# Kernel tuning notes

Hardware: AMD Instinct MI355X
Metric: run time of the kernel (lower is better)

## Reference

```python
import jax, jax.numpy as jnp
import numpy as np

H = 2048        # hidden_size
E = 64          # num_experts
TOPK = 4        # top_k_experts
EPS = 1e-6      # rms_norm_eps
SW = 1024       # sliding_window
NEG = jnp.finfo(jnp.float32).min


def setup_inputs() -> dict:
    key = jax.random.key(0)
    k1, k2, k3, k4, k5 = jax.random.split(key, 5)
    B, S = 2, 4096
    x = jax.random.normal(k1, (B, S, H), jnp.float32)
    # 1-based document ids packed contiguously; 0 = padding
    packed_seq_ids = jnp.sort(jax.random.randint(k2, (B, S), 0, 5), axis=-1)
    # 0 = text, 1/2 = vision tokens
    mm_token_type_ids = jax.random.randint(k3, (B, S), 0, 3)
    scale = jax.random.uniform(k4, (H,), jnp.float32, 0.5, 1.5)
    proj_w = jax.random.normal(k5, (E, H), jnp.float32) * 0.02
    return dict(x=x, packed_seq_ids=packed_seq_ids,
                mm_token_type_ids=mm_token_type_ids, scale=scale, proj_w=proj_w)


def _vision_group_ids(mm):
    # per-image-block ids for vision tokens, -1 for text/padding
    is_v = (mm == 1) | (mm == 2)
    is_prev = jnp.concatenate([jnp.zeros_like(is_v[:, :1]), is_v[:, :-1]], axis=-1)
    starts = is_v & ~is_prev
    gid = jnp.cumsum(starts.astype(jnp.int32), axis=1) - 1
    return jnp.where(is_v, gid, -1)


def _build_masks(packed, mm, sliding_window):
    B, S = packed.shape
    pos = jnp.arange(S)
    causal = pos[None, :, None] >= pos[None, None, :]          # [1,S,S] kv<=q
    valid_q = packed[:, :, None] > 0
    valid_kv = packed[:, None, :] > 0
    same_doc = (packed[:, :, None] == packed[:, None, :]) & valid_q & valid_kv
    full = same_doc & causal                                   # [B,S,S]
    sliding = full & ((pos[None, :, None] - pos[None, None, :]) < sliding_window)
    gid = _vision_group_ids(mm)
    same_vg = (gid[:, :, None] == gid[:, None, :]) & (gid[:, :, None] >= 0)
    sliding = (sliding | same_vg) & same_doc
    # additive format, [B,1,S,S]
    full_add = jnp.where(full[:, None], jnp.float32(0.0), NEG)
    sliding_add = jnp.where(sliding[:, None], jnp.float32(0.0), NEG)
    return full_add, sliding_add


def _gate(x, scale, proj_w):
    # Gemma4Gate: RMSNorm(no scale) -> H**-0.5 -> learnable scale -> linear
    #             -> softmax -> top-k -> renormalize
    xf = x.reshape(-1, H)                                      # [N,H]
    xn = xf * jax.lax.rsqrt(jnp.mean(xf * xf, axis=-1, keepdims=True) + EPS)
    xn = xn * (H ** -0.5) * scale
    logits = jnp.einsum('nh,eh->ne', xn, proj_w)               # [N,E]
    probs = jax.nn.softmax(logits, axis=-1)
    weights, indices = jax.lax.top_k(probs, TOPK)              # [N,K]
    weights = weights / jnp.maximum(jnp.sum(weights, axis=-1, keepdims=True), 1e-20)
    return weights, indices


def reference(x, packed_seq_ids, mm_token_type_ids, scale, proj_w):
    full_mask, sliding_mask = _build_masks(packed_seq_ids, mm_token_type_ids, SW)
    weights, indices = _gate(x, scale, proj_w)
    return full_mask, sliding_mask, weights, indices
```

## Files before the change

### kernel.cpp

```cpp
#include <hip/hip_runtime.h>
#include <math.h>

#define S 4096
#define HH 2048
#define NE 64
#define SW 1024
#define MASKED 0xFBFFu

typedef unsigned short u16;
typedef unsigned int u32;

__device__ __align__(16) int g_gid[2 * S];
__device__ __align__(16) float g_pw2[NE * HH];

__device__ __forceinline__ float h2f(u32 lo16) {
    union { u16 u; _Float16 h; } v; v.u = (u16)lo16; return (float)v.h;
}
__device__ __forceinline__ u16 f2h(float f) {
    union { u16 u; _Float16 h; } v; v.h = (_Float16)f; return v.u;
}
__device__ __forceinline__ void u4_to_f8(uint4 v, float* o) {
    o[0] = h2f(v.x & 0xFFFFu); o[1] = h2f(v.x >> 16);
    o[2] = h2f(v.y & 0xFFFFu); o[3] = h2f(v.y >> 16);
    o[4] = h2f(v.z & 0xFFFFu); o[5] = h2f(v.z >> 16);
    o[6] = h2f(v.w & 0xFFFFu); o[7] = h2f(v.w >> 16);
}

__global__ __launch_bounds__(256) void pre_kernel(const int* __restrict__ mm,
                                                  const u16* __restrict__ proj_w) {
    const int blk = blockIdx.x;
    const int t = threadIdx.x;
    if (blk < 2) {
        __shared__ int ts[256];
        const int* m = mm + blk * S;
        const int base_pos = t * 16;
        int vals[16];
#pragma unroll
        for (int i = 0; i < 16; i++) vals[i] = m[base_pos + i];
        bool prevv = false;
        if (base_pos > 0) {
            int pv = m[base_pos - 1];
            prevv = (pv == 1) || (pv == 2);
        }
        int cnt = 0;
        {
            bool pv = prevv;
#pragma unroll
            for (int i = 0; i < 16; i++) {
                bool is = (vals[i] == 1) || (vals[i] == 2);
                cnt += (is && !pv) ? 1 : 0;
                pv = is;
            }
        }
        ts[t] = cnt;
        __syncthreads();
        for (int off = 1; off < 256; off <<= 1) {
            int add = (t >= off) ? ts[t - off] : 0;
            __syncthreads();
            ts[t] += add;
            __syncthreads();
        }
        int base = ts[t] - cnt;
        {
            bool pv = prevv;
            int run = base;
#pragma unroll
            for (int i = 0; i < 16; i++) {
                bool is = (vals[i] == 1) || (vals[i] == 2);
                run += (is && !pv) ? 1 : 0;
                g_gid[blk * S + base_pos + i] = is ? (run - 1) : -1;
                pv = is;
            }
        }
    } else {
        int idx = (blk - 2) * 256 + t;
        int e = idx >> 11;
        int h = idx & 2047;
        g_pw2[(h >> 2) * 256 + e * 4 + (h & 3)] = h2f((u32)proj_w[idx]);
    }
}

__global__ __launch_bounds__(256) void fused_kernel(
    const u16* __restrict__ x, const u16* __restrict__ scale,
    const int* __restrict__ packed,
    u16* __restrict__ full_out, u16* __restrict__ slid_out,
    u16* __restrict__ w_out, u16* __restrict__ i_out) {

    __shared__ float factor[16];
    __shared__ float xs[16][132];
    __shared__ float part[4][16][65];

    const int t = threadIdx.x;

    if (blockIdx.x >= 512) {
        const int tid = (blockIdx.x - 512) * 256 + t;
        const int kc = tid & 511;
        const int q = (tid >> 9) & 4095;
        const int b = tid >> 21;
        const int k0 = kc * 8;

        const int pq = packed[b * S + q];
        const int gq = g_gid[b * S + q];
        const int4 pk0 = *(const int4*)(packed + b * S + k0);
        const int4 pk1 = *(const int4*)(packed + b * S + k0 + 4);
        const int4 gk0 = *(const int4*)(g_gid + b * S + k0);
        const int4 gk1 = *(const int4*)(g_gid + b * S + k0 + 4);

        int pkj[8] = {pk0.x, pk0.y, pk0.z, pk0.w, pk1.x, pk1.y, pk1.z, pk1.w};
        int gkj[8] = {gk0.x, gk0.y, gk0.z, gk0.w, gk1.x, gk1.y, gk1.z, gk1.w};
        u32 fm[8], sm[8];
#pragma unroll
        for (int j = 0; j < 8; j++) {
            int k = k0 + j;
            bool sd = (pq > 0) && (pkj[j] == pq);
            bool fl = sd && (q >= k);
            bool sl = ((fl && ((q - k) < SW)) || ((gkj[j] == gq) && (gq >= 0))) && sd;
            fm[j] = fl ? 0u : MASKED;
            sm[j] = sl ? 0u : MASKED;
        }
        uint4 f4, s4;
        f4.x = fm[0] | (fm[1] << 16); f4.y = fm[2] | (fm[3] << 16);
        f4.z = fm[4] | (fm[5] << 16); f4.w = fm[6] | (fm[7] << 16);
        s4.x = sm[0] | (sm[1] << 16); s4.y = sm[2] | (sm[3] << 16);
        s4.z = sm[4] | (sm[5] << 16); s4.w = sm[6] | (sm[7] << 16);

        size_t off = (size_t)b * ((size_t)S * S) + (size_t)q * S + k0;
        *(uint4*)(full_out + off) = f4;
        *(uint4*)(slid_out + off) = s4;
        return;
    }

    const int w = t >> 6;
    const int l = t & 63;
    const int tok0 = blockIdx.x * 16;

    for (int tt = w; tt < 16; tt += 4) {
        const uint4* xp = (const uint4*)(x + (size_t)(tok0 + tt) * HH);
        float ss = 0.0f;
#pragma unroll
        for (int j = 0; j < 4; j++) {
            float o[8];
            u4_to_f8(xp[l + 64 * j], o);
#pragma unroll
            for (int i = 0; i < 8; i++) ss += o[i] * o[i];
        }
        for (int off = 32; off >= 1; off >>= 1) ss += __shfl_xor(ss, off);
        if (l == 0)
            factor[tt] = rsqrtf(ss * (1.0f / 2048.0f) + 1e-6f) * 0.022097086912079608f;
    }
    __syncthreads();

    const int g = l & 15;
    const int ts = l >> 4;
    float acc[4][4];
#pragma unroll
    for (int a = 0; a < 4; a++)
#pragma unroll
        for (int bb = 0; bb < 4; bb++) acc[a][bb] = 0.0f;

    const int stok = t >> 4;
    const int sh = (t & 15) * 8;
    const u16* xrow = x + (size_t)(tok0 + stok) * HH + sh;

    uint4 xv_p = *(const uint4*)(xrow);
    uint4 sv_p = *(const uint4*)(scale + sh);

    for (int ch = 0; ch < 16; ch++) {
        __syncthreads();
        {
            float xo[8], so[8];
            u4_to_f8(xv_p, xo);
            u4_to_f8(sv_p, so);
            float fac = factor[stok];
            float4 a, b;
            a.x = xo[0] * fac * so[0]; a.y = xo[1] * fac * so[1];
            a.z = xo[2] * fac * so[2]; a.w = xo[3] * fac * so[3];
            b.x = xo[4] * fac * so[4]; b.y = xo[5] * fac * so[5];
            b.z = xo[6] * fac * so[6]; b.w = xo[7] * fac * so[7];
            *(float4*)&xs[stok][sh] = a;
            *(float4*)&xs[stok][sh + 4] = b;
        }
        __syncthreads();
        if (ch < 15) {
            xv_p = *(const uint4*)(xrow + (ch + 1) * 128);
            sv_p = *(const uint4*)(scale + (ch + 1) * 128 + sh);
        }

        const float* pwb = g_pw2 + (size_t)(ch * 32 + w * 8) * 256 + g * 16;
#pragma unroll
        for (int i = 0; i < 8; i++) {
            float4 p[4];
#pragma unroll
            for (int ej = 0; ej < 4; ej++)
                p[ej] = *(const float4*)(pwb + (size_t)i * 256 + ej * 4);
#pragma unroll
            for (int tk = 0; tk < 4; tk++) {
                float4 xv = *(const float4*)&xs[4 * ts + tk][w * 32 + i * 4];
#pragma unroll
                for (int ej = 0; ej < 4; ej++)
                    acc[tk][ej] += p[ej].x * xv.x + p[ej].y * xv.y +
                                   p[ej].z * xv.z + p[ej].w * xv.w;
            }
        }
    }

#pragma unroll
    for (int tk = 0; tk < 4; tk++)
#pragma unroll
        for (int ej = 0; ej < 4; ej++)
            part[w][4 * ts + tk][4 * g + ej] = acc[tk][ej];
    __syncthreads();

    {
        int tok = t >> 4;
        int eg = t & 15;
        float lg[4];
#pragma unroll
        for (int j = 0; j < 4; j++) {
            int e = eg * 4 + j;
            lg[j] = part[0][tok][e] + part[1][tok][e] + part[2][tok][e] + part[3][tok][e];
        }
        *(float4*)&xs[tok][eg * 4] = make_float4(lg[0], lg[1], lg[2], lg[3]);
    }
    __syncthreads();

    if (t < 16) {
        unsigned long long used = 0ull;
        float bv[4];
        int bi[4];
#pragma unroll
        for (int p = 0; p < 4; p++) {
            float best = -INFINITY;
            int besti = 0;
            for (int e = 0; e < NE; e++) {
                if (used & (1ull << e)) continue;
                float v = xs[t][e];
                if (v > best) { best = v; besti = e; }
            }
            used |= 1ull << besti;
            bv[p] = best;
            bi[p] = besti;
        }
        float ww[4];
        float ssum = 0.0f;
#pragma unroll
        for (int p = 0; p < 4; p++) { ww[p] = expf(bv[p] - bv[0]); ssum += ww[p]; }
        int n = tok0 + t;
#pragma unroll
        for (int p = 0; p < 4; p++) {
            w_out[n * 4 + p] = f2h(ww[p] / ssum);
            i_out[n * 4 + p] = f2h((float)bi[p]);
        }
    }
}

extern "C" void kernel_launch(void* const* d_in, const int* in_sizes, int n_in,
                              void* d_out, int out_size, void* d_ws, size_t ws_size,
                              hipStream_t stream) {
    const u16* x = (const u16*)d_in[0];
    const int* packed = (const int*)d_in[1];
    const int* mm = (const int*)d_in[2];
    const u16* scale = (const u16*)d_in[3];
    const u16* proj_w = (const u16*)d_in[4];

    u16* out = (u16*)d_out;
    u16* full_out = out;
    u16* slid_out = out + 33554432;
    u16* w_out = out + 67108864;
    u16* i_out = out + 67141632;

    pre_kernel<<<514, 256, 0, stream>>>(mm, proj_w);
    fused_kernel<<<512 + 16384, 256, 0, stream>>>(x, scale, packed,
                                                  full_out, slid_out, w_out, i_out);
    (void)in_sizes; (void)n_in; (void)out_size; (void)d_ws; (void)ws_size;
}
```

Measured before the change: 361.5 us.

## Compute gate logits with fp16 MFMA and fold scale into pre-packed weights

The gate GEMM moves from scalar fp32 FMA through shared-memory tiles to 16x16x32 fp16 MFMA instructions, with 64 tokens per block instead of 16. The learnable scale is folded into the projection weights in the pre-kernel, which now stores them as fp16 in an MFMA-friendly B layout. The RMS factor is computed alongside the MFMA loop and applied to the logits afterwards. This removes most shared-memory staging and syncs from the gate path, at the cost of rounding the scaled weights to fp16 and more work per top-k thread. The gate is a small share of the runtime next to the mask writes.

```diff
diff --git a/kernel.cpp b/kernel.cpp
--- a/kernel.cpp
+++ b/kernel.cpp
@@ -9,25 +9,23 @@
 
 typedef unsigned short u16;
 typedef unsigned int u32;
+typedef _Float16 f16;
+typedef f16 f16x8 __attribute__((ext_vector_type(8)));
+typedef float f32x4 __attribute__((ext_vector_type(4)));
 
 __device__ __align__(16) int g_gid[2 * S];
-__device__ __align__(16) float g_pw2[NE * HH];
+__device__ __align__(16) u16 g_pwB[NE * HH];
 
 __device__ __forceinline__ float h2f(u32 lo16) {
-    union { u16 u; _Float16 h; } v; v.u = (u16)lo16; return (float)v.h;
+    union { u16 u; f16 h; } v; v.u = (u16)lo16; return (float)v.h;
 }
 __device__ __forceinline__ u16 f2h(float f) {
-    union { u16 u; _Float16 h; } v; v.h = (_Float16)f; return v.u;
-}
-__device__ __forceinline__ void u4_to_f8(uint4 v, float* o) {
-    o[0] = h2f(v.x & 0xFFFFu); o[1] = h2f(v.x >> 16);
-    o[2] = h2f(v.y & 0xFFFFu); o[3] = h2f(v.y >> 16);
-    o[4] = h2f(v.z & 0xFFFFu); o[5] = h2f(v.z >> 16);
-    o[6] = h2f(v.w & 0xFFFFu); o[7] = h2f(v.w >> 16);
+    union { u16 u; f16 h; } v; v.h = (f16)f; return v.u;
 }
 
 __global__ __launch_bounds__(256) void pre_kernel(const int* __restrict__ mm,
-                                                  const u16* __restrict__ proj_w) {
+                                                  const u16* __restrict__ proj_w,
+                                                  const u16* __restrict__ scale) {
     const int blk = blockIdx.x;
     const int t = threadIdx.x;
     if (blk < 2) {
@@ -76,24 +74,27 @@
         int idx = (blk - 2) * 256 + t;
         int e = idx >> 11;
         int h = idx & 2047;
-        g_pw2[(h >> 2) * 256 + e * 4 + (h & 3)] = h2f((u32)proj_w[idx]);
+        float v = h2f((u32)proj_w[idx]) * h2f((u32)scale[h]);
+        int ch2 = h >> 5;
+        int lrow = (h >> 3) & 3;
+        int j = h & 7;
+        int eg = e >> 4;
+        int ecol = e & 15;
+        g_pwB[(size_t)(((ch2 * 4 + eg) * 64) + lrow * 16 + ecol) * 8 + j] = f2h(v);
     }
 }
 
 __global__ __launch_bounds__(256) void fused_kernel(
-    const u16* __restrict__ x, const u16* __restrict__ scale,
-    const int* __restrict__ packed,
+    const u16* __restrict__ x, const int* __restrict__ packed,
     u16* __restrict__ full_out, u16* __restrict__ slid_out,
     u16* __restrict__ w_out, u16* __restrict__ i_out) {
 
-    __shared__ float factor[16];
-    __shared__ float xs[16][132];
-    __shared__ float part[4][16][65];
+    __shared__ float lg[64][65];
 
     const int t = threadIdx.x;
 
-    if (blockIdx.x >= 512) {
-        const int tid = (blockIdx.x - 512) * 256 + t;
+    if (blockIdx.x >= 128) {
+        const int tid = (blockIdx.x - 128) * 256 + t;
         const int kc = tid & 511;
         const int q = (tid >> 9) & 4095;
         const int b = tid >> 21;
@@ -132,99 +133,54 @@
 
     const int w = t >> 6;
     const int l = t & 63;
-    const int tok0 = blockIdx.x * 16;
-
-    for (int tt = w; tt < 16; tt += 4) {
-        const uint4* xp = (const uint4*)(x + (size_t)(tok0 + tt) * HH);
-        float ss = 0.0f;
-#pragma unroll
-        for (int j = 0; j < 4; j++) {
-            float o[8];
-            u4_to_f8(xp[l + 64 * j], o);
-#pragma unroll
-            for (int i = 0; i < 8; i++) ss += o[i] * o[i];
-        }
-        for (int off = 32; off >= 1; off >>= 1) ss += __shfl_xor(ss, off);
-        if (l == 0)
-            factor[tt] = rsqrtf(ss * (1.0f / 2048.0f) + 1e-6f) * 0.022097086912079608f;
+    const int tok0 = blockIdx.x * 64;
+    const int m16 = l & 15;
+    const int kq = l >> 4;
+
+    const uint4* ap = (const uint4*)(x + (size_t)(tok0 + w * 16 + m16) * HH);
+    const uint4* bp = (const uint4*)g_pwB;
+
+    f32x4 acc0 = {0.f, 0.f, 0.f, 0.f};
+    f32x4 acc1 = {0.f, 0.f, 0.f, 0.f};
+    f32x4 acc2 = {0.f, 0.f, 0.f, 0.f};
+    f32x4 acc3 = {0.f, 0.f, 0.f, 0.f};
+    float ss = 0.0f;
+
+#pragma unroll 4
+    for (int ch2 = 0; ch2 < 64; ++ch2) {
+        union { uint4 u; f16x8 h; } a, b0, b1, b2, b3;
+        a.u = ap[ch2 * 4 + kq];
+        b0.u = bp[(ch2 * 4 + 0) * 64 + l];
+        b1.u = bp[(ch2 * 4 + 1) * 64 + l];
+        b2.u = bp[(ch2 * 4 + 2) * 64 + l];
+        b3.u = bp[(ch2 * 4 + 3) * 64 + l];
+#pragma unroll
+        for (int j = 0; j < 8; j++) {
+            float xf = (float)a.h[j];
+            ss += xf * xf;
+        }
+        acc0 = __builtin_amdgcn_mfma_f32_16x16x32_f16(a.h, b0.h, acc0, 0, 0, 0);
+        acc1 = __builtin_amdgcn_mfma_f32_16x16x32_f16(a.h, b1.h, acc1, 0, 0, 0);
+        acc2 = __builtin_amdgcn_mfma_f32_16x16x32_f16(a.h, b2.h, acc2, 0, 0, 0);
+        acc3 = __builtin_amdgcn_mfma_f32_16x16x32_f16(a.h, b3.h, acc3, 0, 0, 0);
+    }
+
+    ss += __shfl_xor(ss, 16);
+    ss += __shfl_xor(ss, 32);
+    float fac = rsqrtf(ss * (1.0f / 2048.0f) + 1e-6f) * 0.022097086912079608f;
+
+#pragma unroll
+    for (int r = 0; r < 4; r++) {
+        int m = 4 * kq + r;
+        float fm = __shfl(fac, m);
+        lg[w * 16 + m][0 + m16]  = acc0[r] * fm;
+        lg[w * 16 + m][16 + m16] = acc1[r] * fm;
+        lg[w * 16 + m][32 + m16] = acc2[r] * fm;
+        lg[w * 16 + m][48 + m16] = acc3[r] * fm;
     }
     __syncthreads();
 
-    const int g = l & 15;
-    const int ts = l >> 4;
-    float acc[4][4];
-#pragma unroll
-    for (int a = 0; a < 4; a++)
-#pragma unroll
-        for (int bb = 0; bb < 4; bb++) acc[a][bb] = 0.0f;
-
-    const int stok = t >> 4;
-    const int sh = (t & 15) * 8;
-    const u16* xrow = x + (size_t)(tok0 + stok) * HH + sh;
-
-    uint4 xv_p = *(const uint4*)(xrow);
-    uint4 sv_p = *(const uint4*)(scale + sh);
-
-    for (int ch = 0; ch < 16; ch++) {
-        __syncthreads();
-        {
-            float xo[8], so[8];
-            u4_to_f8(xv_p, xo);
-            u4_to_f8(sv_p, so);
-            float fac = factor[stok];
-            float4 a, b;
-            a.x = xo[0] * fac * so[0]; a.y = xo[1] * fac * so[1];
-            a.z = xo[2] * fac * so[2]; a.w = xo[3] * fac * so[3];
-            b.x = xo[4] * fac * so[4]; b.y = xo[5] * fac * so[5];
-            b.z = xo[6] * fac * so[6]; b.w = xo[7] * fac * so[7];
-            *(float4*)&xs[stok][sh] = a;
-            *(float4*)&xs[stok][sh + 4] = b;
-        }
-        __syncthreads();
-        if (ch < 15) {
-            xv_p = *(const uint4*)(xrow + (ch + 1) * 128);
-            sv_p = *(const uint4*)(scale + (ch + 1) * 128 + sh);
-        }
-
-        const float* pwb = g_pw2 + (size_t)(ch * 32 + w * 8) * 256 + g * 16;
-#pragma unroll
-        for (int i = 0; i < 8; i++) {
-            float4 p[4];
-#pragma unroll
-            for (int ej = 0; ej < 4; ej++)
-                p[ej] = *(const float4*)(pwb + (size_t)i * 256 + ej * 4);
-#pragma unroll
-            for (int tk = 0; tk < 4; tk++) {
-                float4 xv = *(const float4*)&xs[4 * ts + tk][w * 32 + i * 4];
-#pragma unroll
-                for (int ej = 0; ej < 4; ej++)
-                    acc[tk][ej] += p[ej].x * xv.x + p[ej].y * xv.y +
-                                   p[ej].z * xv.z + p[ej].w * xv.w;
-            }
-        }
-    }
-
-#pragma unroll
-    for (int tk = 0; tk < 4; tk++)
-#pragma unroll
-        for (int ej = 0; ej < 4; ej++)
-            part[w][4 * ts + tk][4 * g + ej] = acc[tk][ej];
-    __syncthreads();
-
-    {
-        int tok = t >> 4;
-        int eg = t & 15;
-        float lg[4];
-#pragma unroll
-        for (int j = 0; j < 4; j++) {
-            int e = eg * 4 + j;
-            lg[j] = part[0][tok][e] + part[1][tok][e] + part[2][tok][e] + part[3][tok][e];
-        }
-        *(float4*)&xs[tok][eg * 4] = make_float4(lg[0], lg[1], lg[2], lg[3]);
-    }
-    __syncthreads();
-
-    if (t < 16) {
+    if (t < 64) {
         unsigned long long used = 0ull;
         float bv[4];
         int bi[4];
@@ -234,7 +190,7 @@
             int besti = 0;
             for (int e = 0; e < NE; e++) {
                 if (used & (1ull << e)) continue;
-                float v = xs[t][e];
+                float v = lg[t][e];
                 if (v > best) { best = v; besti = e; }
             }
             used |= 1ull << besti;
@@ -269,8 +225,8 @@
     u16* w_out = out + 67108864;
     u16* i_out = out + 67141632;
 
-    pre_kernel<<<514, 256, 0, stream>>>(mm, proj_w);
-    fused_kernel<<<512 + 16384, 256, 0, stream>>>(x, scale, packed,
+    pre_kernel<<<514, 256, 0, stream>>>(mm, proj_w, scale);
+    fused_kernel<<<128 + 16384, 256, 0, stream>>>(x, packed,
                                                   full_out, slid_out, w_out, i_out);
     (void)in_sizes; (void)n_in; (void)out_size; (void)d_ws; (void)ws_size;
 }
```

Result: faster. 308.7 us (median of 2 runs) (-14.6%).
